# Performance work log

Hardware: AMD Instinct MI355X
Metric: run time of the kernel (lower is better)

## Reference

```python
import jax, jax.numpy as jnp
import numpy as np

# Module hyperparameters (from init_kwargs)
MANHATTAN_WEIGHTS = jnp.asarray([1.0, 1.0, 2.0], dtype=jnp.float32)  # per-xyz weights
R = 0.4       # density radius
ALPHA = 1.0   # density exponent


def setup_inputs() -> dict:
    key = jax.random.key(0)
    k1, k2 = jax.random.split(key)
    B, N, C = 4, 8192, 16
    points = jax.random.normal(k1, (B, N, 3), dtype=jnp.float32)
    features = jax.random.normal(k2, (B, C, N), dtype=jnp.float32)
    return {"points": points, "features": features, "npoint": 2048}


def reference(points, features, npoint):
    """Density + Manhattan weighted furthest point sampling.

    points:   [B, N, 3] xyz coordinates
    features: [B, C, N] (unused by the sampler, kept for API parity)
    returns:  [B, npoint] int32 sampled indices
    """
    B, N, _ = points.shape
    w = MANHATTAN_WEIGHTS.astype(points.dtype)

    # Per-point density: number of neighbors within Euclidean radius R. [B, N]
    d2 = jnp.sum((points[:, :, None, :] - points[:, None, :, :]) ** 2, axis=-1)  # [B,N,N]
    density = jnp.sum(d2 <= R * R, axis=-1).astype(points.dtype)  # >= 1 (includes self)
    penalty = density ** (-ALPHA)  # low-density points get boosted distance

    def step(carry, _):
        min_dist, cur = carry  # [B,N], [B]
        # coordinates of most recently selected point: [B, 1, 3]
        p = jnp.take_along_axis(points, cur[:, None, None].astype(jnp.int32), axis=1)
        # weighted Manhattan distance of every point to the new sample: [B, N]
        d = jnp.sum(w * jnp.abs(points - p), axis=-1)
        min_dist = jnp.minimum(min_dist, d)
        # fused density-weighted furthest-point criterion
        nxt = jnp.argmax(min_dist * penalty, axis=-1).astype(jnp.int32)
        return (min_dist, nxt), cur

    init = (jnp.full((B, N), 1e10, dtype=points.dtype), jnp.zeros((B,), dtype=jnp.int32))
    _, idx = jax.lax.scan(step, init, None, length=npoint)  # idx: [npoint, B]
    return jnp.transpose(idx)  # [B, npoint]
```

## Files before the change

kernel.cpp:

```cpp
#include <hip/hip_runtime.h>


#define NPTS 8192
#define DENS_BLOCK 256
#define DENS_SPLIT 2
#define FPS_THREADS 512
#define FPS_P 16
#define NWAVES (FPS_THREADS / 64)


__global__ void dfps_density_partial(const float* __restrict__ pts,
                                     float* __restrict__ pen, int N) {
#pragma clang fp contract(off)
    const float R2 = (float)(0.4 * 0.4);
    const int b = blockIdx.y;
    const int z = blockIdx.z;
    const int i = blockIdx.x * blockDim.x + threadIdx.x;
    const float* P = pts + (size_t)b * N * 3;

    __shared__ float4 tile[DENS_BLOCK];

    const float px = P[i * 3 + 0], py = P[i * 3 + 1], pz = P[i * 3 + 2];
    const int half = N / DENS_SPLIT;
    const int j0 = z * half;

    int cnt = 0;
    for (int t0 = j0; t0 < j0 + half; t0 += DENS_BLOCK) {
        int j = t0 + threadIdx.x;
        __syncthreads();
        tile[threadIdx.x] = make_float4(P[j * 3 + 0], P[j * 3 + 1], P[j * 3 + 2], 0.f);
        __syncthreads();
        for (int jj = 0; jj < DENS_BLOCK; ++jj) {
            float4 q = tile[jj];
            float dx = px - q.x, dy = py - q.y, dz = pz - q.z;
            float d2 = dx * dx;
            d2 = d2 + dy * dy;
            d2 = d2 + dz * dz;
            cnt += (d2 <= R2) ? 1 : 0;
        }
    }
    atomicAdd(&pen[(size_t)b * N + i], (float)cnt);
}

__global__ void dfps_finalize(float* pen, int total) {
    int i = blockIdx.x * blockDim.x + threadIdx.x;
    if (i < total) pen[i] = 1.0f / pen[i];
}


#define DPP_STEP(ctrl, rmask)                                                   \
    {                                                                           \
        unsigned int nlo = (unsigned int)__builtin_amdgcn_update_dpp(           \
            0, (int)klo, (ctrl), (rmask), 0xF, false);                          \
        unsigned int nhi = (unsigned int)__builtin_amdgcn_update_dpp(           \
            0, (int)khi, (ctrl), (rmask), 0xF, false);                          \
        unsigned long long o = ((unsigned long long)nhi << 32) | nlo;           \
        unsigned long long c = ((unsigned long long)khi << 32) | klo;           \
        if (o > c) { klo = nlo; khi = nhi; }                                    \
    }

__global__ void __launch_bounds__(FPS_THREADS, 1)
dfps_fps_kernel(const float* __restrict__ pts,
                const float* __restrict__ penalty,
                const int* __restrict__ npoint_p,
                int* __restrict__ out, int N) {
#pragma clang fp contract(off)
    const int b = blockIdx.x;
    const int tid = threadIdx.x;
    const int lane = tid & 63;
    const int w = tid >> 6;
    const int npoint = *npoint_p;
    const float* Pb = pts + (size_t)b * N * 3;
    const float* pen = penalty + (size_t)b * N;
    const int base = tid * FPS_P;

    __shared__ float slx[NPTS], sly[NPTS], slz[NPTS];
    __shared__ unsigned long long kbuf[2][NWAVES];

    float x[FPS_P], y[FPS_P], z[FPS_P], md[FPS_P], pw[FPS_P];
    unsigned int lo[FPS_P];
#pragma unroll
    for (int k = 0; k < FPS_P; ++k) {
        int idx = base + k;
        x[k] = Pb[idx * 3 + 0];
        y[k] = Pb[idx * 3 + 1];
        z[k] = Pb[idx * 3 + 2];
        md[k] = 1e10f;
        pw[k] = pen[idx];
        lo[k] = (unsigned int)(N - 1 - idx);
        slx[idx] = x[k];
        sly[idx] = y[k];
        slz[idx] = z[k];
    }

    int cur = 0;
    float cx = Pb[0], cy = Pb[1], cz = Pb[2];

    for (int t = 0; t < npoint; ++t) {
        if (tid == 0) out[(size_t)b * npoint + t] = cur;

        unsigned long long ck0 = 0ull, ck1 = 0ull, ck2 = 0ull, ck3 = 0ull;
#pragma unroll
        for (int k = 0; k < FPS_P; ++k) {
            float d = fabsf(x[k] - cx) + fabsf(y[k] - cy);
            d = fmaf(2.0f, fabsf(z[k] - cz), d);
            float m = fminf(md[k], d);
            md[k] = m;
            float v = m * pw[k];
            unsigned long long key =
                ((unsigned long long)__float_as_uint(v) << 32) | lo[k];
            if ((k & 3) == 0)      { if (key > ck0) ck0 = key; }
            else if ((k & 3) == 1) { if (key > ck1) ck1 = key; }
            else if ((k & 3) == 2) { if (key > ck2) ck2 = key; }
            else                   { if (key > ck3) ck3 = key; }
        }
        unsigned long long ka = ck0 > ck1 ? ck0 : ck1;
        unsigned long long kb = ck2 > ck3 ? ck2 : ck3;
        unsigned long long best = ka > kb ? ka : kb;

        unsigned int klo = (unsigned int)best;
        unsigned int khi = (unsigned int)(best >> 32);
        DPP_STEP(0x111, 0xF)
        DPP_STEP(0x112, 0xF)
        DPP_STEP(0x114, 0xF)
        DPP_STEP(0x118, 0xF)
        DPP_STEP(0x142, 0xA)
        DPP_STEP(0x143, 0xC)
        unsigned int wlo = (unsigned int)__builtin_amdgcn_readlane((int)klo, 63);
        unsigned int whi = (unsigned int)__builtin_amdgcn_readlane((int)khi, 63);

        if (lane == 0)
            kbuf[t & 1][w] = ((unsigned long long)whi << 32) | wlo;
        __syncthreads();

        unsigned long long b0 = kbuf[t & 1][0], b1 = kbuf[t & 1][1];
        unsigned long long b2 = kbuf[t & 1][2], b3 = kbuf[t & 1][3];
        unsigned long long b4 = kbuf[t & 1][4], b5 = kbuf[t & 1][5];
        unsigned long long b6 = kbuf[t & 1][6], b7 = kbuf[t & 1][7];
        b0 = b0 > b1 ? b0 : b1;
        b2 = b2 > b3 ? b2 : b3;
        b4 = b4 > b5 ? b4 : b5;
        b6 = b6 > b7 ? b6 : b7;
        b0 = b0 > b2 ? b0 : b2;
        b4 = b4 > b6 ? b4 : b6;
        b0 = b0 > b4 ? b0 : b4;

        cur = (N - 1) - (int)(unsigned int)(b0 & 0xFFFFFFFFull);
        cx = slx[cur];
        cy = sly[cur];
        cz = slz[cur];
    }
}

extern "C" void kernel_launch(void* const* d_in, const int* in_sizes, int n_in,
                              void* d_out, int out_size, void* d_ws, size_t ws_size,
                              hipStream_t stream) {
    const float* points  = (const float*)d_in[0];
    const int*   npoint  = (const int*)d_in[2];
    int* out = (int*)d_out;

    const int B = 4;
    const int N = in_sizes[0] / (B * 3);
    float* penalty = (float*)d_ws;

    hipMemsetAsync(penalty, 0, (size_t)B * N * sizeof(float), stream);

    dim3 dgrid(N / DENS_BLOCK, B, DENS_SPLIT);
    dfps_density_partial<<<dgrid, DENS_BLOCK, 0, stream>>>(points, penalty, N);
    dfps_finalize<<<(B * N + 255) / 256, 256, 0, stream>>>(penalty, B * N);

    dfps_fps_kernel<<<B, FPS_THREADS, 0, stream>>>(points, penalty, npoint, out, N);
}
```

Measured before the change: 2.030 ms.

## Use LDS atomicMax triple-buffer slot for cross-wave argmax and fuse density finalize

Each wave's lane 63 now does an LDS 64-bit atomicMax into a rotating triple-buffered slot, replacing the per-wave key buffer and the eight-way serial reduction after the barrier. The next slot is zeroed ahead of time so one barrier per iteration is enough. Point coordinates are stored as one float4 table so the selected point is fetched with a single LDS load. The density kernel drops the two-way split, the memset and the atomics, and writes the reciprocal count directly, which removes two launches but halves density-kernel parallelism.

```diff
diff --git a/kernel.cpp b/kernel.cpp
--- a/kernel.cpp
+++ b/kernel.cpp
@@ -3,48 +3,42 @@
 
 #define NPTS 8192
 #define DENS_BLOCK 256
-#define DENS_SPLIT 2
 #define FPS_THREADS 512
 #define FPS_P 16
-#define NWAVES (FPS_THREADS / 64)
 
 
-__global__ void dfps_density_partial(const float* __restrict__ pts,
-                                     float* __restrict__ pen, int N) {
+__global__ void dfps_density_kernel(const float* __restrict__ pts,
+                                    float* __restrict__ pen, int N) {
 #pragma clang fp contract(off)
     const float R2 = (float)(0.4 * 0.4);
     const int b = blockIdx.y;
-    const int z = blockIdx.z;
     const int i = blockIdx.x * blockDim.x + threadIdx.x;
     const float* P = pts + (size_t)b * N * 3;
 
-    __shared__ float4 tile[DENS_BLOCK];
+    __shared__ float sx[DENS_BLOCK], sy[DENS_BLOCK], sz[DENS_BLOCK];
 
     const float px = P[i * 3 + 0], py = P[i * 3 + 1], pz = P[i * 3 + 2];
-    const int half = N / DENS_SPLIT;
-    const int j0 = z * half;
 
     int cnt = 0;
-    for (int t0 = j0; t0 < j0 + half; t0 += DENS_BLOCK) {
+    for (int t0 = 0; t0 < N; t0 += DENS_BLOCK) {
         int j = t0 + threadIdx.x;
         __syncthreads();
-        tile[threadIdx.x] = make_float4(P[j * 3 + 0], P[j * 3 + 1], P[j * 3 + 2], 0.f);
+        sx[threadIdx.x] = P[j * 3 + 0];
+        sy[threadIdx.x] = P[j * 3 + 1];
+        sz[threadIdx.x] = P[j * 3 + 2];
         __syncthreads();
+#pragma unroll 4
         for (int jj = 0; jj < DENS_BLOCK; ++jj) {
-            float4 q = tile[jj];
-            float dx = px - q.x, dy = py - q.y, dz = pz - q.z;
+            float dx = px - sx[jj];
+            float dy = py - sy[jj];
+            float dz = pz - sz[jj];
             float d2 = dx * dx;
             d2 = d2 + dy * dy;
             d2 = d2 + dz * dz;
             cnt += (d2 <= R2) ? 1 : 0;
         }
     }
-    atomicAdd(&pen[(size_t)b * N + i], (float)cnt);
-}
-
-__global__ void dfps_finalize(float* pen, int total) {
-    int i = blockIdx.x * blockDim.x + threadIdx.x;
-    if (i < total) pen[i] = 1.0f / pen[i];
+    pen[(size_t)b * N + i] = 1.0f / (float)cnt;
 }
 
 
@@ -68,14 +62,13 @@
     const int b = blockIdx.x;
     const int tid = threadIdx.x;
     const int lane = tid & 63;
-    const int w = tid >> 6;
     const int npoint = *npoint_p;
     const float* Pb = pts + (size_t)b * N * 3;
     const float* pen = penalty + (size_t)b * N;
     const int base = tid * FPS_P;
 
-    __shared__ float slx[NPTS], sly[NPTS], slz[NPTS];
-    __shared__ unsigned long long kbuf[2][NWAVES];
+    __shared__ float4 tab[NPTS];
+    __shared__ unsigned long long slot[3];
 
     float x[FPS_P], y[FPS_P], z[FPS_P], md[FPS_P], pw[FPS_P];
     unsigned int lo[FPS_P];
@@ -88,16 +81,19 @@
         md[k] = 1e10f;
         pw[k] = pen[idx];
         lo[k] = (unsigned int)(N - 1 - idx);
-        slx[idx] = x[k];
-        sly[idx] = y[k];
-        slz[idx] = z[k];
+        tab[idx] = make_float4(x[k], y[k], z[k], 0.f);
     }
+    if (tid == 0) { slot[0] = 0ull; slot[2] = 0ull; }
+    __syncthreads();
 
     int cur = 0;
     float cx = Pb[0], cy = Pb[1], cz = Pb[2];
 
     for (int t = 0; t < npoint; ++t) {
-        if (tid == 0) out[(size_t)b * npoint + t] = cur;
+        if (tid == 0) {
+            out[(size_t)b * npoint + t] = cur;
+            slot[(t + 1) % 3] = 0ull;
+        }
 
         unsigned long long ck0 = 0ull, ck1 = 0ull, ck2 = 0ull, ck3 = 0ull;
 #pragma unroll
@@ -126,29 +122,19 @@
         DPP_STEP(0x118, 0xF)
         DPP_STEP(0x142, 0xA)
         DPP_STEP(0x143, 0xC)
-        unsigned int wlo = (unsigned int)__builtin_amdgcn_readlane((int)klo, 63);
-        unsigned int whi = (unsigned int)__builtin_amdgcn_readlane((int)khi, 63);
 
-        if (lane == 0)
-            kbuf[t & 1][w] = ((unsigned long long)whi << 32) | wlo;
+        if (lane == 63) {
+            unsigned long long wk = ((unsigned long long)khi << 32) | klo;
+            atomicMax(&slot[t % 3], wk);
+        }
         __syncthreads();
 
-        unsigned long long b0 = kbuf[t & 1][0], b1 = kbuf[t & 1][1];
-        unsigned long long b2 = kbuf[t & 1][2], b3 = kbuf[t & 1][3];
-        unsigned long long b4 = kbuf[t & 1][4], b5 = kbuf[t & 1][5];
-        unsigned long long b6 = kbuf[t & 1][6], b7 = kbuf[t & 1][7];
-        b0 = b0 > b1 ? b0 : b1;
-        b2 = b2 > b3 ? b2 : b3;
-        b4 = b4 > b5 ? b4 : b5;
-        b6 = b6 > b7 ? b6 : b7;
-        b0 = b0 > b2 ? b0 : b2;
-        b4 = b4 > b6 ? b4 : b6;
-        b0 = b0 > b4 ? b0 : b4;
-
-        cur = (N - 1) - (int)(unsigned int)(b0 & 0xFFFFFFFFull);
-        cx = slx[cur];
-        cy = sly[cur];
-        cz = slz[cur];
+        unsigned long long bk = slot[t % 3];
+        cur = (N - 1) - (int)(unsigned int)(bk & 0xFFFFFFFFull);
+        float4 c = tab[cur];
+        cx = c.x;
+        cy = c.y;
+        cz = c.z;
     }
 }
 
@@ -163,11 +149,8 @@
     const int N = in_sizes[0] / (B * 3);
     float* penalty = (float*)d_ws;
 
-    hipMemsetAsync(penalty, 0, (size_t)B * N * sizeof(float), stream);
-
-    dim3 dgrid(N / DENS_BLOCK, B, DENS_SPLIT);
-    dfps_density_partial<<<dgrid, DENS_BLOCK, 0, stream>>>(points, penalty, N);
-    dfps_finalize<<<(B * N + 255) / 256, 256, 0, stream>>>(penalty, B * N);
+    dim3 dgrid(N / DENS_BLOCK, B);
+    dfps_density_kernel<<<dgrid, DENS_BLOCK, 0, stream>>>(points, penalty, N);
 
     dfps_fps_kernel<<<B, FPS_THREADS, 0, stream>>>(points, penalty, npoint, out, N);
 }
```

After: 2.051 ms. Within noise of the previous version (+1.0%).
